# Kernel optimization log

Hardware: AMD Instinct MI355X
Metric: run time of the kernel (lower is better)

## Reference

```python
import jax, jax.numpy as jnp
import numpy as np

MINING_MARGIN = 0.1
MARGIN = 0.3
EPS = 1e-6  # torch F.pairwise_distance adds eps to the elementwise difference


def _normalize(v):
    # torch F.normalize(p=2): v / max(||v||, 1e-12)
    n = jnp.linalg.norm(v, axis=-1, keepdims=True)
    return v / jnp.maximum(n, 1e-12)


def setup_inputs() -> dict:
    key = jax.random.key(0)
    x = jax.random.normal(key, (16384, 2, 256), dtype=jnp.float32)
    return {"x": x}


def reference(x):
    a = _normalize(x[:, 0, :])  # [B, D] anchors
    p = _normalize(x[:, 1, :])  # [B, D] positives
    # mining uses detached embeddings
    ad = jax.lax.stop_gradient(a)
    pd = jax.lax.stop_gradient(p)
    B, d = ad.shape

    # Full pairwise distance matrix D[i, j] = ||ad[i] - pd[j] + EPS||_2,
    # expanded algebraically to avoid a [B, B, D] intermediate:
    # ||a - p + e||^2 = ||a||^2 + ||p||^2 - 2 a.p + 2e*(sum(a) - sum(p)) + d*e^2
    dot = ad @ pd.T                                   # [B, B]
    na2 = jnp.sum(ad * ad, axis=1)                    # [B]
    np2 = jnp.sum(pd * pd, axis=1)                    # [B]
    sa = jnp.sum(ad, axis=1)                          # [B]
    sp = jnp.sum(pd, axis=1)                          # [B]
    D2 = (na2[:, None] + np2[None, :] - 2.0 * dot
          + 2.0 * EPS * (sa[:, None] - sp[None, :]) + d * EPS * EPS)
    D = jnp.sqrt(jnp.clip(D2, 0.0))                   # [B, B]

    diag = jnp.diagonal(D)                            # anchor-to-own-positive dist
    # semihard: farther than positive but within mining_margin
    mask = (D > diag[:, None]) & (D < diag[:, None] + MINING_MARGIN)

    # GPU-side uniform random choice per row among masked candidates
    k1, k2 = jax.random.split(jax.random.key(1))
    g = jax.random.uniform(k1, (B, B))
    scores = jnp.where(mask, g, -1.0)
    cand = jnp.argmax(scores, axis=1)                 # random masked index
    fallback = jax.random.randint(k2, (B,), 0, B)     # random.choice(posidx)
    negidx = jnp.where(jnp.any(mask, axis=1), cand, fallback)

    neg = p[negidx]                                   # [B, D]
    pos_dist = jnp.linalg.norm(a - p + EPS, axis=1)
    neg_dist = jnp.linalg.norm(a - neg + EPS, axis=1)
    loss = jnp.mean(jax.nn.relu(pos_dist ** 2 - neg_dist ** 2 + MARGIN))
    return loss
```

## Files before the change

kernel.cpp:

```cpp
#include <hip/hip_runtime.h>
#include <stdint.h>

#define B_N 16384
#define DIMV 256
#define XSTRIDE 512
#define EPSF 1e-6f
#define CEF 2.56e-10f
#define TWOEPS 2e-6f
#define MINING 0.1f
#define MARGINF 0.3f
#define NSTRIP 8

typedef __attribute__((ext_vector_type(8))) short bf16x8;
typedef __attribute__((ext_vector_type(4))) float f32x4;

__device__ __forceinline__ void tf2x32(uint32_t k0, uint32_t k1,
                                       uint32_t& x0, uint32_t& x1) {
  uint32_t k2 = k0 ^ k1 ^ 0x1BD11BDAu;
  x0 += k0; x1 += k1;
#define TFR(r) { x0 += x1; x1 = (x1 << (r)) | (x1 >> (32 - (r))); x1 ^= x0; }
  TFR(13) TFR(15) TFR(26) TFR(6)
  x0 += k1; x1 += k2 + 1u;
  TFR(17) TFR(29) TFR(16) TFR(24)
  x0 += k2; x1 += k0 + 2u;
  TFR(13) TFR(15) TFR(26) TFR(6)
  x0 += k0; x1 += k1 + 3u;
  TFR(17) TFR(29) TFR(16) TFR(24)
  x0 += k1; x1 += k2 + 4u;
  TFR(13) TFR(15) TFR(26) TFR(6)
  x0 += k2; x1 += k0 + 5u;
#undef TFR
}

#define TF_ROT(x, r) __builtin_amdgcn_alignbit((x), (x), 32u - (r))

__device__ __forceinline__ uint32_t tf_mb(uint32_t K0, uint32_t K1, uint32_t c1) {
  const uint32_t K2 = K0 ^ K1 ^ 0x1BD11BDAu;
  uint32_t x0 = K0;
  uint32_t x1 = c1 + K1;
#define R4A { x0 += x1; x1 = TF_ROT(x1, 13); x1 ^= x0; \
              x0 += x1; x1 = TF_ROT(x1, 15); x1 ^= x0; \
              x0 += x1; x1 = TF_ROT(x1, 26); x1 ^= x0; \
              x0 += x1; x1 = TF_ROT(x1, 6);  x1 ^= x0; }
#define R4B { x0 += x1; x1 = TF_ROT(x1, 17); x1 ^= x0; \
              x0 += x1; x1 = TF_ROT(x1, 29); x1 ^= x0; \
              x0 += x1; x1 = TF_ROT(x1, 16); x1 ^= x0; \
              x0 += x1; x1 = TF_ROT(x1, 24); x1 ^= x0; }
  R4A; x0 += K1; x1 += K2 + 1u;
  R4B; x0 += K2; x1 += K0 + 2u;
  R4A; x0 += K0; x1 += K1 + 3u;
  R4B; x0 += K1; x1 += K2 + 4u;
  R4A; x0 += K2; x1 += K0 + 5u;
#undef R4A
#undef R4B
  return (x0 ^ x1) >> 9;
}

__device__ __forceinline__ float wave_sum(float v) {
#pragma unroll
  for (int off = 32; off > 0; off >>= 1) v += __shfl_xor(v, off, 64);
  return v;
}

__device__ __forceinline__ void gl_lds16(const unsigned short* g, unsigned short* s) {
  __builtin_amdgcn_global_load_lds(
      (const __attribute__((address_space(1))) void*)g,
      (__attribute__((address_space(3))) void*)s, 16, 0, 0);
}

__device__ __forceinline__ uint32_t split_pack(float v) {
  const uint32_t u = __float_as_uint(v);
  const uint32_t hi = (u + 0x7FFFu + ((u >> 16) & 1u)) >> 16;
  const float hf = __uint_as_float(hi << 16);
  const float lf = v - hf;
  const uint32_t ul = __float_as_uint(lf);
  const uint32_t lo = (ul + 0x7FFFu + ((ul >> 16) & 1u)) >> 16;
  return hi | (lo << 16);
}

__global__ void k1_stats(const float* __restrict__ x, float* __restrict__ invA,
                         float* __restrict__ invP, float* __restrict__ rowA,
                         float* __restrict__ colB, float* __restrict__ lo,
                         float* __restrict__ pos2) {
  const int i = blockIdx.x;
  const int l = threadIdx.x;
  const float4 va = *(const float4*)&x[i * XSTRIDE + l * 4];
  const float4 vp = *(const float4*)&x[i * XSTRIDE + DIMV + l * 4];
  float saa = va.x*va.x + va.y*va.y + va.z*va.z + va.w*va.w;
  float spp = vp.x*vp.x + vp.y*vp.y + vp.z*vp.z + vp.w*vp.w;
  saa = wave_sum(saa); spp = wave_sum(spp);
  const float ia = 1.0f / fmaxf(sqrtf(saa), 1e-12f);
  const float ip = 1.0f / fmaxf(sqrtf(spp), 1e-12f);
  const float ax = va.x*ia, ay = va.y*ia, az = va.z*ia, aw = va.w*ia;
  const float px = vp.x*ip, py = vp.y*ip, pz = vp.z*ip, pw = vp.w*ip;
  float na2 = ax*ax + ay*ay + az*az + aw*aw;
  float np2 = px*px + py*py + pz*pz + pw*pw;
  float sa  = ax + ay + az + aw;
  float sp  = px + py + pz + pw;
  float dii = ax*px + ay*py + az*pz + aw*pw;
  const float dx = ax-px+EPSF, dy = ay-py+EPSF, dz = az-pz+EPSF, dw = aw-pw+EPSF;
  float ps = dx*dx + dy*dy + dz*dz + dw*dw;
  na2 = wave_sum(na2); np2 = wave_sum(np2); sa = wave_sum(sa);
  sp  = wave_sum(sp);  dii = wave_sum(dii); ps = wave_sum(ps);
  if (l == 0) {
    const float rA = na2 + TWOEPS * sa + CEF;
    const float cB = np2 - TWOEPS * sp;
    invA[i] = ia; invP[i] = ip; rowA[i] = rA; colB[i] = cB;
    lo[i] = sqrtf(fmaxf(rA + cB - 2.0f * dii, 0.0f));
    pos2[i] = ps;
  }
}

__global__ void k1b_cvt(const float* __restrict__ x, const float* __restrict__ invA,
                        const float* __restrict__ invP,
                        unsigned short* __restrict__ Abf,
                        unsigned short* __restrict__ Pbf) {
  const int t = blockIdx.x * 256 + threadIdx.x;
  const int row = t >> 6, l = t & 63;
  const float ia = invA[row], ip = invP[row];
  const float4 va = *(const float4*)&x[row * XSTRIDE + l * 4];
  const float4 vp = *(const float4*)&x[row * XSTRIDE + DIMV + l * 4];
  uint4 oa, op;
  oa.x = split_pack(va.x * ia); oa.y = split_pack(va.y * ia);
  oa.z = split_pack(va.z * ia); oa.w = split_pack(va.w * ia);
  op.x = split_pack(vp.x * ip); op.y = split_pack(vp.y * ip);
  op.z = split_pack(vp.z * ip); op.w = split_pack(vp.w * ip);
  *(uint4*)&Abf[(size_t)row * 512 + l * 8] = oa;
  *(uint4*)&Pbf[(size_t)row * 512 + l * 8] = op;
}

__global__ __launch_bounds__(256, 2) void k2_mfma(
    const unsigned short* __restrict__ Abf, const unsigned short* __restrict__ Pbf,
    const float* __restrict__ rowA, const float* __restrict__ colB,
    const float* __restrict__ lo, unsigned long long* __restrict__ partials) {
  __shared__ __align__(16) unsigned short As[64 * 64];
  __shared__ __align__(16) unsigned short Bs[128 * 64];

  const int tid = threadIdx.x;
  const int w = tid >> 6;
  const int l = tid & 63;
  const int q = l >> 4;
  const int c16 = l & 15;
  const int rBase = blockIdx.x * 64;
  const int strip = blockIdx.y;

  uint32_t K0 = 0u, K1 = 0u;
  tf2x32(0u, 1u, K0, K1);

  const int sw = c16 & 7;
  const int sgk = (l & 7) ^ ((l >> 3) & 7);

  const int arow = rBase + w * 16 + (l >> 3);
  const unsigned short* gA0 = Abf + (size_t)arow * 512 + sgk * 8;
  unsigned short* lA0 = &As[(w * 16) * 64];
  unsigned short* lB0 = &Bs[(w * 32) * 64];

  float Lr[4], Hr[4];
  const int iBase = rBase + w * 16 + q * 4;
#pragma unroll
  for (int ri = 0; ri < 4; ++ri) {
    const int i = iBase + ri;
    const float ra = rowA[i];
    const float lv = lo[i];
    Lr[ri] = lv * lv - ra;
    Hr[ri] = (lv + MINING) * (lv + MINING) - ra;
  }

  int bmb[4], bj[4];
#pragma unroll
  for (int ri = 0; ri < 4; ++ri) { bmb[ri] = -1; bj[ri] = 0; }

  for (int ct = 0; ct < 16; ++ct) {
    const int cBase = strip * 2048 + ct * 128;
    const int brow = cBase + w * 32 + (l >> 3);
    const unsigned short* gB0 = Pbf + (size_t)brow * 512 + sgk * 8;

    f32x4 acc[8];
#pragma unroll
    for (int n = 0; n < 8; ++n) {
      f32x4 z = {0.0f, 0.0f, 0.0f, 0.0f};
      acc[n] = z;
    }

    for (int kc = 0; kc < 512; kc += 64) {
      __syncthreads();
#pragma unroll
      for (int u = 0; u < 2; ++u)
        gl_lds16(gA0 + kc + u * 8 * 512, lA0 + u * 8 * 64);
#pragma unroll
      for (int u = 0; u < 4; ++u)
        gl_lds16(gB0 + kc + u * 8 * 512, lB0 + u * 8 * 64);
      __syncthreads();
#pragma unroll
      for (int ks = 0; ks < 2; ++ks) {
        const int px = ((ks * 4 + q) ^ sw) * 8;
        const bf16x8 am = *(const bf16x8*)&As[(w * 16 + c16) * 64 + px];
        bf16x8 bn[8];
#pragma unroll
        for (int n = 0; n < 8; ++n)
          bn[n] = *(const bf16x8*)&Bs[(n * 16 + c16) * 64 + px];
#pragma unroll
        for (int n = 0; n < 8; ++n)
          acc[n] = __builtin_amdgcn_mfma_f32_16x16x32_bf16(am, bn[n], acc[n],
                                                           0, 0, 0);
      }
    }

#pragma unroll
    for (int n = 0; n < 8; ++n) {
      const int j = cBase + n * 16 + c16;
      const float cb = colB[j];
#pragma unroll
      for (int ri = 0; ri < 4; ++ri) {
        const int i = iBase + ri;
        const float t = fmaf(-2.0f, acc[n][ri], cb);
        const uint32_t mb = tf_mb(K0, K1, ((uint32_t)i << 14) | (uint32_t)j);
        const bool upd = (t > Lr[ri]) & (t < Hr[ri]) & (j != i) &
                         ((int)mb > bmb[ri]);
        bmb[ri] = upd ? (int)mb : bmb[ri];
        bj[ri]  = upd ? j : bj[ri];
      }
    }
  }

#pragma unroll
  for (int ri = 0; ri < 4; ++ri) {
    unsigned long long bk = 0ull;
    if (bmb[ri] >= 0)
      bk = ((unsigned long long)(uint32_t)(bmb[ri] + 1) << 32) |
           (unsigned long long)(uint32_t)(16383 - bj[ri]);
#pragma unroll
    for (int off = 1; off < 16; off <<= 1) {
      const unsigned long long o = __shfl_xor(bk, off, 64);
      if (o > bk) bk = o;
    }
    if (c16 == 0)
      partials[(size_t)(iBase + ri) * NSTRIP + strip] = bk;
  }
}

#define TM 64
#define TN 128
#define KC 64
#define AS_LD 68
#define BS_LD 132
#define COLS_PER_STRIP (B_N / NSTRIP)
#define TILES_PER_STRIP (COLS_PER_STRIP / TN)

__global__ __launch_bounds__(256, 3) void k2_mine(
    const float* __restrict__ x, const float* __restrict__ invA,
    const float* __restrict__ invP, const float* __restrict__ rowA,
    const float* __restrict__ colB, const float* __restrict__ lo,
    unsigned long long* __restrict__ partials) {
  __shared__ __align__(16) float As[KC * AS_LD];
  __shared__ __align__(16) float Bs[KC * BS_LD];
  __shared__ float colBs[TN];

  const int tid = threadIdx.x;
  const int ty = tid >> 4;
  const int tx = tid & 15;
  const int rBase = blockIdx.x * TM;
  const int strip = blockIdx.y;
  const int cStart = strip * COLS_PER_STRIP;

  uint32_t k1h = 0u, k1l = 0u;
  tf2x32(0u, 1u, k1h, k1l);

  float rowA_r[4], lo_r[4];
  int rows[4];
#pragma unroll
  for (int m = 0; m < 4; ++m) {
    rows[m] = rBase + ty * 4 + m;
    rowA_r[m] = rowA[rows[m]];
    lo_r[m] = lo[rows[m]];
  }

  unsigned long long best[4] = {0ull, 0ull, 0ull, 0ull};
  const int skq = tid & 15;
  const int srr = tid >> 4;

  for (int ct = 0; ct < TILES_PER_STRIP; ++ct) {
    const int cBase = cStart + ct * TN;
    float acc[4][8];
#pragma unroll
    for (int m = 0; m < 4; ++m)
#pragma unroll
      for (int n = 0; n < 8; ++n) acc[m][n] = 0.0f;

    for (int kc = 0; kc < DIMV; kc += KC) {
      __syncthreads();
#pragma unroll
      for (int u = 0; u < 4; ++u) {
        const int r = srr + 16 * u;
        const int row = rBase + r;
        const float4 v = *(const float4*)&x[row * XSTRIDE + kc + skq * 4];
        const float s = invA[row];
        As[(skq * 4 + 0) * AS_LD + r] = v.x * s;
        As[(skq * 4 + 1) * AS_LD + r] = v.y * s;
        As[(skq * 4 + 2) * AS_LD + r] = v.z * s;
        As[(skq * 4 + 3) * AS_LD + r] = v.w * s;
      }
#pragma unroll
      for (int u = 0; u < 8; ++u) {
        const int c = srr + 16 * u;
        const int col = cBase + c;
        const float4 v = *(const float4*)&x[col * XSTRIDE + DIMV + kc + skq * 4];
        const float s = invP[col];
        Bs[(skq * 4 + 0) * BS_LD + c] = v.x * s;
        Bs[(skq * 4 + 1) * BS_LD + c] = v.y * s;
        Bs[(skq * 4 + 2) * BS_LD + c] = v.z * s;
        Bs[(skq * 4 + 3) * BS_LD + c] = v.w * s;
      }
      if (kc == 0 && tid < TN) colBs[tid] = colB[cBase + tid];
      __syncthreads();

#pragma unroll 8
      for (int k = 0; k < KC; ++k) {
        const float4 a4 = *(const float4*)&As[k * AS_LD + ty * 4];
        const float4 bl = *(const float4*)&Bs[k * BS_LD + tx * 4];
        const float4 bh = *(const float4*)&Bs[k * BS_LD + 64 + tx * 4];
        const float am[4] = {a4.x, a4.y, a4.z, a4.w};
        const float bn[8] = {bl.x, bl.y, bl.z, bl.w, bh.x, bh.y, bh.z, bh.w};
#pragma unroll
        for (int m = 0; m < 4; ++m)
#pragma unroll
          for (int n = 0; n < 8; ++n)
            acc[m][n] = fmaf(am[m], bn[n], acc[m][n]);
      }
    }

#pragma unroll
    for (int m = 0; m < 4; ++m) {
      const int i = rows[m];
      const float loi = lo_r[m];
      const float hii = loi + MINING;
#pragma unroll
      for (int n = 0; n < 8; ++n) {
        const int cOff = (n < 4) ? (tx * 4 + n) : (64 + tx * 4 + (n - 4));
        const int j = cBase + cOff;
        const float D2 = rowA_r[m] + colBs[cOff] - 2.0f * acc[m][n];
        const float D = sqrtf(fmaxf(D2, 0.0f));
        if (D > loi && D < hii && j != i) {
          uint32_t c0 = 0u;
          uint32_t c1 = ((uint32_t)i << 14) | (uint32_t)j;
          tf2x32(k1h, k1l, c0, c1);
          const uint32_t bits = c0 ^ c1;
          const uint32_t mb = bits >> 9;
          const unsigned long long pk =
              ((unsigned long long)(mb + 1u) << 32) |
              (unsigned long long)(uint32_t)(16383 - j);
          if (pk > best[m]) best[m] = pk;
        }
      }
    }
  }

  __syncthreads();
  unsigned long long* red = (unsigned long long*)As;
#pragma unroll
  for (int m = 0; m < 4; ++m) red[(ty * 4 + m) * 16 + tx] = best[m];
  __syncthreads();
  if (tid < TM) {
    unsigned long long g = red[tid * 16];
#pragma unroll
    for (int t = 1; t < 16; ++t) {
      const unsigned long long v = red[tid * 16 + t];
      if (v > g) g = v;
    }
    partials[(size_t)(rBase + tid) * NSTRIP + strip] = g;
  }
}

__global__ void k3_select(const unsigned long long* __restrict__ partials,
                          int* __restrict__ negidx) {
  const int i = blockIdx.x * 256 + threadIdx.x;
  unsigned long long g = 0ull;
#pragma unroll
  for (int s = 0; s < NSTRIP; ++s) {
    const unsigned long long v = partials[(size_t)i * NSTRIP + s];
    if (v > g) g = v;
  }
  int ng;
  if (g != 0ull) {
    ng = 16383 - (int)(g & 0xFFFFFFFFull);
  } else {
    uint32_t t0 = 0u, t1 = 1u;
    tf2x32(0u, 1u, t0, t1);
    uint32_t u0 = 0u, u1 = 1u;
    tf2x32(t0, t1, u0, u1);
    uint32_t v0 = 0u, v1 = (uint32_t)i;
    tf2x32(u0, u1, v0, v1);
    ng = (int)((v0 ^ v1) & 16383u);
  }
  negidx[i] = ng;
}

__global__ void k4_loss(const float* __restrict__ x, const float* __restrict__ invA,
                        const float* __restrict__ invP, const float* __restrict__ pos2,
                        const int* __restrict__ negidx, float* __restrict__ bsums) {
  const int w = threadIdx.x >> 6;
  const int l = threadIdx.x & 63;
  const int i = blockIdx.x * 4 + w;
  const float ia = invA[i];
  const int ng = negidx[i];
  const float ip = invP[ng];
  const float4 va = *(const float4*)&x[i * XSTRIDE + l * 4];
  const float4 vn = *(const float4*)&x[ng * XSTRIDE + DIMV + l * 4];
  const float dx = va.x * ia - vn.x * ip + EPSF;
  const float dy = va.y * ia - vn.y * ip + EPSF;
  const float dz = va.z * ia - vn.z * ip + EPSF;
  const float dw = va.w * ia - vn.w * ip + EPSF;
  float s = dx*dx + dy*dy + dz*dz + dw*dw;
  s = wave_sum(s);
  __shared__ float bs[4];
  if (l == 0) bs[w] = fmaxf(pos2[i] - s + MARGINF, 0.0f);
  __syncthreads();
  if (threadIdx.x == 0) bsums[blockIdx.x] = bs[0] + bs[1] + bs[2] + bs[3];
}

__global__ void k5_reduce(const float* __restrict__ bsums, float* __restrict__ out) {
  float s = 0.0f;
  for (int idx = threadIdx.x; idx < (B_N / 4); idx += 256) s += bsums[idx];
  s = wave_sum(s);
  __shared__ float acc4[4];
  if ((threadIdx.x & 63) == 0) acc4[threadIdx.x >> 6] = s;
  __syncthreads();
  if (threadIdx.x == 0)
    out[0] = (acc4[0] + acc4[1] + acc4[2] + acc4[3]) * (1.0f / (float)B_N);
}

extern "C" void kernel_launch(void* const* d_in, const int* in_sizes, int n_in,
                              void* d_out, int out_size, void* d_ws, size_t ws_size,
                              hipStream_t stream) {
  const float* x = (const float*)d_in[0];
  char* ws = (char*)d_ws;
  size_t off = 0;
  unsigned long long* partials = (unsigned long long*)(ws + off);
  off += (size_t)B_N * NSTRIP * sizeof(unsigned long long);
  float* invA = (float*)(ws + off); off += (size_t)B_N * 4;
  float* invP = (float*)(ws + off); off += (size_t)B_N * 4;
  float* rowA = (float*)(ws + off); off += (size_t)B_N * 4;
  float* colB = (float*)(ws + off); off += (size_t)B_N * 4;
  float* lo   = (float*)(ws + off); off += (size_t)B_N * 4;
  float* pos2 = (float*)(ws + off); off += (size_t)B_N * 4;
  int* negidx = (int*)(ws + off);   off += (size_t)B_N * 4;
  float* bsums = (float*)(ws + off); off += (size_t)(B_N / 4) * 4;
  unsigned short* Abf = (unsigned short*)(ws + off);
  off += (size_t)B_N * 512 * sizeof(unsigned short);
  unsigned short* Pbf = (unsigned short*)(ws + off);
  off += (size_t)B_N * 512 * sizeof(unsigned short);
  const size_t ws_need = off;
  float* out = (float*)d_out;

  hipLaunchKernelGGL(k1_stats, dim3(B_N), dim3(64), 0, stream,
                     x, invA, invP, rowA, colB, lo, pos2);
  if (ws_size >= ws_need) {
    hipLaunchKernelGGL(k1b_cvt, dim3(B_N / 4), dim3(256), 0, stream,
                       x, invA, invP, Abf, Pbf);
    hipLaunchKernelGGL(k2_mfma, dim3(B_N / 64, NSTRIP), dim3(256), 0, stream,
                       Abf, Pbf, rowA, colB, lo, partials);
  } else {
    hipLaunchKernelGGL(k2_mine, dim3(B_N / TM, NSTRIP), dim3(256), 0, stream,
                       x, invA, invP, rowA, colB, lo, partials);
  }
  hipLaunchKernelGGL(k3_select, dim3(B_N / 256), dim3(256), 0, stream,
                     partials, negidx);
  hipLaunchKernelGGL(k4_loss, dim3(B_N / 4), dim3(256), 0, stream,
                     x, invA, invP, pos2, negidx, bsums);
  hipLaunchKernelGGL(k5_reduce, dim3(1), dim3(256), 0, stream, bsums, out);
}
```

Measured before the change: 826.1 us.

## Compact semihard candidates via ballot queue before computing threefry randoms

Per-element threefry evaluation during mining is replaced by a wave-level stream compaction. Candidates that pass the semihard mask are written to an LDS queue using ballot and mbcnt prefix counts. Only the queued entries then get a random key, which is reduced into per-row LDS slots with 64-bit atomicMax. This is meant to avoid the costly RNG on the large majority of pairs that fail the mask, at the price of LDS traffic, divergence and LDS atomics.

```diff
diff --git a/kernel.cpp b/kernel.cpp
--- a/kernel.cpp
+++ b/kernel.cpp
@@ -135,6 +135,8 @@
     const float* __restrict__ lo, unsigned long long* __restrict__ partials) {
   __shared__ __align__(16) unsigned short As[64 * 64];
   __shared__ __align__(16) unsigned short Bs[128 * 64];
+  __shared__ uint32_t qbuf[4][256];
+  __shared__ unsigned long long slots[4][16];
 
   const int tid = threadIdx.x;
   const int w = tid >> 6;
@@ -155,6 +157,8 @@
   unsigned short* lA0 = &As[(w * 16) * 64];
   unsigned short* lB0 = &Bs[(w * 32) * 64];
 
+  if (l < 16) slots[w][l] = 0ull;
+
   float Lr[4], Hr[4];
   const int iBase = rBase + w * 16 + q * 4;
 #pragma unroll
@@ -166,9 +170,7 @@
     Hr[ri] = (lv + MINING) * (lv + MINING) - ra;
   }
 
-  int bmb[4], bj[4];
-#pragma unroll
-  for (int ri = 0; ri < 4; ++ri) { bmb[ri] = -1; bj[ri] = 0; }
+  uint32_t qn = 0;
 
   for (int ct = 0; ct < 16; ++ct) {
     const int cBase = strip * 2048 + ct * 128;
@@ -214,29 +216,29 @@
       for (int ri = 0; ri < 4; ++ri) {
         const int i = iBase + ri;
         const float t = fmaf(-2.0f, acc[n][ri], cb);
-        const uint32_t mb = tf_mb(K0, K1, ((uint32_t)i << 14) | (uint32_t)j);
-        const bool upd = (t > Lr[ri]) & (t < Hr[ri]) & (j != i) &
-                         ((int)mb > bmb[ri]);
-        bmb[ri] = upd ? (int)mb : bmb[ri];
-        bj[ri]  = upd ? j : bj[ri];
-      }
-    }
-  }
-
-#pragma unroll
-  for (int ri = 0; ri < 4; ++ri) {
-    unsigned long long bk = 0ull;
-    if (bmb[ri] >= 0)
-      bk = ((unsigned long long)(uint32_t)(bmb[ri] + 1) << 32) |
-           (unsigned long long)(uint32_t)(16383 - bj[ri]);
-#pragma unroll
-    for (int off = 1; off < 16; off <<= 1) {
-      const unsigned long long o = __shfl_xor(bk, off, 64);
-      if (o > bk) bk = o;
-    }
-    if (c16 == 0)
-      partials[(size_t)(iBase + ri) * NSTRIP + strip] = bk;
-  }
+        const bool pred = (t > Lr[ri]) & (t < Hr[ri]) & (j != i);
+        const unsigned long long bal = __ballot(pred);
+        uint32_t pre = __builtin_amdgcn_mbcnt_lo((uint32_t)bal, 0u);
+        pre = __builtin_amdgcn_mbcnt_hi((uint32_t)(bal >> 32), pre);
+        if (pred) qbuf[w][qn + pre] = ((uint32_t)i << 14) | (uint32_t)j;
+        qn += (uint32_t)__popcll(bal);
+      }
+      asm volatile("s_waitcnt lgkmcnt(0)" ::: "memory");
+      for (uint32_t k = (uint32_t)l; k < qn; k += 64u) {
+        const uint32_t cand = qbuf[w][k];
+        const uint32_t mb = tf_mb(K0, K1, cand);
+        const unsigned long long key =
+            ((unsigned long long)(mb + 1u) << 32) |
+            (unsigned long long)(16383u - (cand & 16383u));
+        atomicMax(&slots[w][(cand >> 14) & 15u], key);
+      }
+      qn = 0;
+    }
+  }
+
+  asm volatile("s_waitcnt lgkmcnt(0)" ::: "memory");
+  if (l < 16)
+    partials[(size_t)(rBase + w * 16 + l) * NSTRIP + strip] = slots[w][l];
 }
 
 #define TM 64
```

New measurement: 846.6 us. +2.5%, slower.

## Split mining into MFMA bitmap pass and sparse random-draw pass

Applied to the files above, without the earlier changes.

The fused MFMA mining kernel now only writes a ballot bitmap of semihard candidates per 64x2048 tile. A second kernel walks the set bits and evaluates the threefry random draw only for masked pairs, using LDS atomicMax per row. This is meant to take the per-element RNG cost out of the dense GEMM epilogue. In exchange it adds a 32 MB bitmap write and read, an extra launch, and load imbalance that depends on mask density. It runs only when the workspace is large enough.

```diff
diff --git a/kernel.cpp b/kernel.cpp
--- a/kernel.cpp
+++ b/kernel.cpp
@@ -129,7 +129,143 @@
   *(uint4*)&Pbf[(size_t)row * 512 + l * 8] = op;
 }
 
-__global__ __launch_bounds__(256, 2) void k2_mfma(
+__global__ __launch_bounds__(256, 2) void k2_mfma_bm(
+    const unsigned short* __restrict__ Abf, const unsigned short* __restrict__ Pbf,
+    const float* __restrict__ rowA, const float* __restrict__ colB,
+    const float* __restrict__ lo, unsigned long long* __restrict__ bitmap) {
+  __shared__ __align__(16) unsigned short As[64 * 64];
+  __shared__ __align__(16) unsigned short Bs[128 * 64];
+
+  const int tid = threadIdx.x;
+  const int w = tid >> 6;
+  const int l = tid & 63;
+  const int q = l >> 4;
+  const int c16 = l & 15;
+  const int rBase = blockIdx.x * 64;
+  const int strip = blockIdx.y;
+
+  const int sw = c16 & 7;
+  const int sgk = (l & 7) ^ ((l >> 3) & 7);
+
+  const int arow = rBase + w * 16 + (l >> 3);
+  const unsigned short* gA0 = Abf + (size_t)arow * 512 + sgk * 8;
+  unsigned short* lA0 = &As[(w * 16) * 64];
+  unsigned short* lB0 = &Bs[(w * 32) * 64];
+
+  unsigned long long* wordsBlk =
+      bitmap + ((size_t)blockIdx.x * NSTRIP + strip) * 2048;
+
+  float Lr[4], Hr[4];
+  const int iBase = rBase + w * 16 + q * 4;
+#pragma unroll
+  for (int ri = 0; ri < 4; ++ri) {
+    const int i = iBase + ri;
+    const float ra = rowA[i];
+    const float lv = lo[i];
+    Lr[ri] = lv * lv - ra;
+    Hr[ri] = (lv + MINING) * (lv + MINING) - ra;
+  }
+
+  for (int ct = 0; ct < 16; ++ct) {
+    const int cBase = strip * 2048 + ct * 128;
+    const int brow = cBase + w * 32 + (l >> 3);
+    const unsigned short* gB0 = Pbf + (size_t)brow * 512 + sgk * 8;
+
+    f32x4 acc[8];
+#pragma unroll
+    for (int n = 0; n < 8; ++n) {
+      f32x4 z = {0.0f, 0.0f, 0.0f, 0.0f};
+      acc[n] = z;
+    }
+
+    for (int kc = 0; kc < 512; kc += 64) {
+      __syncthreads();
+#pragma unroll
+      for (int u = 0; u < 2; ++u)
+        gl_lds16(gA0 + kc + u * 8 * 512, lA0 + u * 8 * 64);
+#pragma unroll
+      for (int u = 0; u < 4; ++u)
+        gl_lds16(gB0 + kc + u * 8 * 512, lB0 + u * 8 * 64);
+      __syncthreads();
+#pragma unroll
+      for (int ks = 0; ks < 2; ++ks) {
+        const int px = ((ks * 4 + q) ^ sw) * 8;
+        const bf16x8 am = *(const bf16x8*)&As[(w * 16 + c16) * 64 + px];
+        bf16x8 bn[8];
+#pragma unroll
+        for (int n = 0; n < 8; ++n)
+          bn[n] = *(const bf16x8*)&Bs[(n * 16 + c16) * 64 + px];
+#pragma unroll
+        for (int n = 0; n < 8; ++n)
+          acc[n] = __builtin_amdgcn_mfma_f32_16x16x32_bf16(am, bn[n], acc[n],
+                                                           0, 0, 0);
+      }
+    }
+
+#pragma unroll
+    for (int n = 0; n < 8; ++n) {
+      const int j = cBase + n * 16 + c16;
+      const float cb = colB[j];
+#pragma unroll
+      for (int ri = 0; ri < 4; ++ri) {
+        const int i = iBase + ri;
+        const float t = fmaf(-2.0f, acc[n][ri], cb);
+        const bool pred = (t > Lr[ri]) & (t < Hr[ri]) & (j != i);
+        const unsigned long long bal = __ballot(pred);
+        if (l == 0)
+          wordsBlk[((w * 16 + ct) * 8 + n) * 4 + ri] = bal;
+      }
+    }
+  }
+}
+
+__global__ __launch_bounds__(256, 4) void k3b_draw(
+    const unsigned long long* __restrict__ bitmap,
+    unsigned long long* __restrict__ partials) {
+  __shared__ unsigned long long slots[64];
+  const int tid = threadIdx.x;
+  const int rt = blockIdx.x, strip = blockIdx.y;
+  if (tid < 64) slots[tid] = 0ull;
+  __syncthreads();
+
+  uint32_t K0 = 0u, K1 = 0u;
+  tf2x32(0u, 1u, K0, K1);
+
+  const unsigned long long* wordsBlk =
+      bitmap + ((size_t)rt * NSTRIP + strip) * 2048;
+  const int rowBase = rt * 64;
+  const int colBase = strip * 2048;
+
+  unsigned long long bits = 0ull;
+  int wiCur = 0;
+  int wiNext = tid;
+  for (;;) {
+    while (bits == 0ull && wiNext < 2048) {
+      bits = wordsBlk[wiNext];
+      wiCur = wiNext;
+      wiNext += 256;
+    }
+    if (bits == 0ull) break;
+    const int b = __ffsll(bits) - 1;
+    bits &= bits - 1ull;
+    const int ri = wiCur & 3;
+    const int n  = (wiCur >> 2) & 7;
+    const int ct = (wiCur >> 5) & 15;
+    const int w  = wiCur >> 9;
+    const int i = rowBase + w * 16 + (b >> 4) * 4 + ri;
+    const int j = colBase + ct * 128 + n * 16 + (b & 15);
+    const uint32_t mb = tf_mb(K0, K1, ((uint32_t)i << 14) | (uint32_t)j);
+    const unsigned long long key =
+        ((unsigned long long)(mb + 1u) << 32) |
+        (unsigned long long)(uint32_t)(16383 - j);
+    atomicMax(&slots[i & 63], key);
+  }
+  __syncthreads();
+  if (tid < 64)
+    partials[(size_t)(rowBase + tid) * NSTRIP + strip] = slots[tid];
+}
+
+__global__ __launch_bounds__(256, 2) void k2_mfma_dense(
     const unsigned short* __restrict__ Abf, const unsigned short* __restrict__ Pbf,
     const float* __restrict__ rowA, const float* __restrict__ colB,
     const float* __restrict__ lo, unsigned long long* __restrict__ partials) {
@@ -449,16 +585,26 @@
   off += (size_t)B_N * 512 * sizeof(unsigned short);
   unsigned short* Pbf = (unsigned short*)(ws + off);
   off += (size_t)B_N * 512 * sizeof(unsigned short);
-  const size_t ws_need = off;
+  const size_t ws_need_bf16 = off;
+  unsigned long long* bitmap = (unsigned long long*)(ws + off);
+  off += (size_t)2048 * 2048 * sizeof(unsigned long long);
+  const size_t ws_need_bitmap = off;
   float* out = (float*)d_out;
 
   hipLaunchKernelGGL(k1_stats, dim3(B_N), dim3(64), 0, stream,
                      x, invA, invP, rowA, colB, lo, pos2);
-  if (ws_size >= ws_need) {
+  if (ws_size >= ws_need_bitmap) {
     hipLaunchKernelGGL(k1b_cvt, dim3(B_N / 4), dim3(256), 0, stream,
                        x, invA, invP, Abf, Pbf);
-    hipLaunchKernelGGL(k2_mfma, dim3(B_N / 64, NSTRIP), dim3(256), 0, stream,
-                       Abf, Pbf, rowA, colB, lo, partials);
+    hipLaunchKernelGGL(k2_mfma_bm, dim3(B_N / 64, NSTRIP), dim3(256), 0, stream,
+                       Abf, Pbf, rowA, colB, lo, bitmap);
+    hipLaunchKernelGGL(k3b_draw, dim3(B_N / 64, NSTRIP), dim3(256), 0, stream,
+                       bitmap, partials);
+  } else if (ws_size >= ws_need_bf16) {
+    hipLaunchKernelGGL(k1b_cvt, dim3(B_N / 4), dim3(256), 0, stream,
+                       x, invA, invP, Abf, Pbf);
+    hipLaunchKernelGGL(k2_mfma_dense, dim3(B_N / 64, NSTRIP), dim3(256), 0,
+                       stream, Abf, Pbf, rowA, colB, lo, partials);
   } else {
     hipLaunchKernelGGL(k2_mine, dim3(B_N / TM, NSTRIP), dim3(256), 0, stream,
                        x, invA, invP, rowA, colB, lo, partials);
```

Result: slower. 960.1 us (+16.2%).
